# Optimization experiments

Hardware: AMD Instinct MI355X
Metric: run time of the kernel (lower is better)

Reference implementation:

```python
import jax, jax.numpy as jnp
import numpy as np

N, E, B, L = 20000, 320000, 64, 4
DIN_SEQ, DIN_STR, HID = 1280, 128, 256
NHEAD, HDIM = 8, 32
EPS = 1e-5
SLOPE = 0.2


def setup_inputs() -> dict:
    key = jax.random.key(0)
    ks = iter(jax.random.split(key, 64))
    def nrm(shape, scale=0.05):
        return jax.random.normal(next(ks), shape, dtype=jnp.float32) * scale
    return {
        "seq_x": jax.random.normal(next(ks), (N, DIN_SEQ), dtype=jnp.float32),
        "struct_x": jax.random.normal(next(ks), (N, DIN_STR), dtype=jnp.float32),
        "seq_edge_index": jax.random.randint(next(ks), (2, E), 0, N),
        "struct_edge_index": jax.random.randint(next(ks), (2, E), 0, N),
        "seq_batch": jnp.sort(jax.random.randint(next(ks), (N,), 0, B)),
        "struct_batch": jnp.sort(jax.random.randint(next(ks), (N,), 0, B)),
        "seq_proj_W": nrm((DIN_SEQ, HID)), "seq_proj_b": nrm((HID,)),
        "gcn_W": nrm((L, HID, HID)), "gcn_b": nrm((L, HID)),
        "seq_bn_g": jnp.ones((L, HID), jnp.float32), "seq_bn_b": jnp.zeros((L, HID), jnp.float32),
        "struct_proj_W": nrm((DIN_STR, HID)), "struct_proj_b": nrm((HID,)),
        "gat_W": nrm((L, HID, HID)), "gat_att_src": nrm((L, NHEAD, HDIM)),
        "gat_att_dst": nrm((L, NHEAD, HDIM)), "gat_b": nrm((L, HID)),
        "struct_bn_g": jnp.ones((L, HID), jnp.float32), "struct_bn_b": jnp.zeros((L, HID), jnp.float32),
        "Wq": nrm((HID, HID)), "bq": nrm((HID,)),
        "Wk": nrm((HID, HID)), "bk": nrm((HID,)),
        "Wv": nrm((HID, HID)), "bv": nrm((HID,)),
        "Wo": nrm((HID, HID)), "bo": nrm((HID,)),
        "fus_W": nrm((2 * HID, HID)), "fus_b": nrm((HID,)),
        "p1_W": nrm((HID, HID // 2)), "p1_b": nrm((HID // 2,)),
        "p2_W": nrm((HID // 2, 1)), "p2_b": nrm((1,)),
    }


def _add_self_loops(edge_index, n):
    loops = jnp.arange(n, dtype=edge_index.dtype)
    return jnp.concatenate([edge_index[0], loops]), jnp.concatenate([edge_index[1], loops])


def _batchnorm(x, g, b):
    # PyG BatchNorm forward (training-mode batch stats, biased variance, eps=1e-5)
    mu = x.mean(axis=0)
    var = x.var(axis=0)
    return g * (x - mu) * jax.lax.rsqrt(var + EPS) + b


def _gcn(x, src, dst, W, b):
    # GCNConv: symmetric-normalized gather -> scatter-add, self loops already appended
    n = x.shape[0]
    deg = jax.ops.segment_sum(jnp.ones_like(src, dtype=x.dtype), dst, num_segments=n)
    dinv = jax.lax.rsqrt(jnp.maximum(deg, 1.0))
    h = x @ W
    msg = h[src] * (dinv[src] * dinv[dst])[:, None]
    return jax.ops.segment_sum(msg, dst, num_segments=n) + b


def _seg_softmax(e, dst, n):
    m = jax.ops.segment_max(e, dst, num_segments=n)
    ex = jnp.exp(e - m[dst])
    s = jax.ops.segment_sum(ex, dst, num_segments=n)
    return ex / s[dst]


def _gat(x, src, dst, W, a_src, a_dst, b):
    # GATConv: per-edge LeakyReLU attention, softmax over incoming edges, concat heads
    n = x.shape[0]
    h = (x @ W).reshape(n, NHEAD, HDIM)
    e = jax.nn.leaky_relu((h * a_src).sum(-1)[src] + (h * a_dst).sum(-1)[dst], SLOPE)  # [E,H]
    alpha = _seg_softmax(e, dst, n)
    out = jax.ops.segment_sum(h[src] * alpha[:, :, None], dst, num_segments=n)
    return out.reshape(n, NHEAD * HDIM) + b


def _mean_pool(x, batch, nb):
    s = jax.ops.segment_sum(x, batch, num_segments=nb)
    c = jax.ops.segment_sum(jnp.ones((x.shape[0],), x.dtype), batch, num_segments=nb)
    return s / jnp.maximum(c, 1.0)[:, None]


def reference(seq_x, struct_x, seq_edge_index, struct_edge_index, seq_batch, struct_batch,
              seq_proj_W, seq_proj_b, gcn_W, gcn_b, seq_bn_g, seq_bn_b,
              struct_proj_W, struct_proj_b, gat_W, gat_att_src, gat_att_dst, gat_b,
              struct_bn_g, struct_bn_b, Wq, bq, Wk, bk, Wv, bv, Wo, bo,
              fus_W, fus_b, p1_W, p1_b, p2_W, p2_b):
    s_src, s_dst = _add_self_loops(seq_edge_index, seq_x.shape[0])
    t_src, t_dst = _add_self_loops(struct_edge_index, struct_x.shape[0])
    # sequence branch: GCN stack
    xs = jax.nn.relu(seq_x @ seq_proj_W + seq_proj_b)
    for l in range(gcn_W.shape[0]):
        xs = jax.nn.relu(_batchnorm(_gcn(xs, s_src, s_dst, gcn_W[l], gcn_b[l]), seq_bn_g[l], seq_bn_b[l]))
    xs = _mean_pool(xs, seq_batch, B)  # [B, HID]
    # structure branch: GAT stack
    xt = jax.nn.relu(struct_x @ struct_proj_W + struct_proj_b)
    for l in range(gat_W.shape[0]):
        xt = jax.nn.relu(_batchnorm(_gat(xt, t_src, t_dst, gat_W[l], gat_att_src[l], gat_att_dst[l], gat_b[l]), struct_bn_g[l], struct_bn_b[l]))
    xt = _mean_pool(xt, struct_batch, B)  # [B, HID]
    # cross-attention with query/key/value seq-len 1 (softmax over singleton axis)
    q = (xs @ Wq + bq).reshape(B, NHEAD, HDIM)
    k = (xt @ Wk + bk).reshape(B, NHEAD, HDIM)
    v = (xt @ Wv + bv).reshape(B, NHEAD, HDIM)
    scores = (q * k).sum(-1, keepdims=True) * (1.0 / np.sqrt(HDIM))  # [B,H,1]
    attn = jax.nn.softmax(scores, axis=-1)
    x_attn = (attn * v).reshape(B, HID) @ Wo + bo
    # fusion + predictor (dropout inactive at inference)
    xf = jax.nn.relu(jnp.concatenate([x_attn, xt], axis=1) @ fus_W + fus_b)
    h = jax.nn.relu(xf @ p1_W + p1_b)
    return h @ p2_W + p2_b  # [B, 1]
```

## Files before the change

### kernel.cpp

```cpp
#include <hip/hip_runtime.h>
#include <math.h>

#define NN 20000
#define NE 320000
#define NTOT (NE + NN)
#define NBATCH 64
#define HIDW 256
#define NHEADS 8
#define HD 32
#define NL 4
#define BEPS 1e-5f
#define LSLOPE 0.2f
#define WELEMS (128 * HIDW + NL * HIDW * HIDW)

typedef __attribute__((ext_vector_type(8))) short s16x8;
typedef __attribute__((ext_vector_type(8))) unsigned short u16x8;
typedef __attribute__((ext_vector_type(4))) float f32x4;

static __device__ __forceinline__ ushort f2bf(float f) {
  uint u = __float_as_uint(f);
  uint r = (u + 0x7fff + ((u >> 16) & 1)) >> 16;
  return (ushort)r;
}
static __device__ __forceinline__ float bf2f(ushort h) {
  return __uint_as_float(((uint)h) << 16);
}

__global__ __launch_bounds__(1024) void k_scan(const int* __restrict__ cnt,
                                               int* __restrict__ rowptr) {
  __shared__ int tsum[1024];
  int tid = threadIdx.x;
  const int per = (NN + 1023) / 1024;
  int start = tid * per;
  int local = 0;
  for (int j = 0; j < per; ++j) {
    int idx = start + j;
    if (idx < NN) local += cnt[idx];
  }
  tsum[tid] = local;
  __syncthreads();
  for (int off = 1; off < 1024; off <<= 1) {
    int v = (tid >= off) ? tsum[tid - off] : 0;
    __syncthreads();
    tsum[tid] += v;
    __syncthreads();
  }
  int run = (tid == 0) ? 0 : tsum[tid - 1];
  for (int j = 0; j < per; ++j) {
    int idx = start + j;
    if (idx < NN) { rowptr[idx] = run; run += cnt[idx]; }
  }
  if (tid == 1023) rowptr[NN] = tsum[1023];
}

__global__ void k_fill(const int* __restrict__ src, const int* __restrict__ dst,
                       const int* __restrict__ rowptr, int* __restrict__ cur,
                       int* __restrict__ srcs) {
  int i = blockIdx.x * blockDim.x + threadIdx.x;
  if (i >= NTOT) return;
  int s = (i < NE) ? src[i] : (i - NE);
  int d = (i < NE) ? dst[i] : (i - NE);
  int pos = rowptr[d] + atomicAdd(&cur[d], 1);
  srcs[pos] = s;
}

#define WB ((WELEMS + 255) / 256)
#define XB ((NN * 128 / 4 + 255) / 256)
#define HB ((NTOT + 255) / 256)
__global__ __launch_bounds__(256) void k_prep(const float* __restrict__ projW,
                                              const float* __restrict__ gatW,
                                              const float* __restrict__ sx,
                                              const int* __restrict__ e_dst,
                                              ushort* __restrict__ wh,
                                              ushort* __restrict__ sxh,
                                              int* __restrict__ cnt) {
  int bb = blockIdx.x;
  if (bb < WB) {
    int i = bb * 256 + threadIdx.x;
    if (i >= WELEMS) return;
    float v;
    if (i < 128 * HIDW) {
      int n = i >> 7, k = i & 127;
      v = projW[k * HIDW + n];
    } else {
      int j = i - 128 * HIDW;
      int l = j >> 16, r = j & 65535;
      int n = r >> 8, k = r & 255;
      v = gatW[l * 65536 + k * HIDW + n];
    }
    wh[i] = f2bf(v);
  } else if (bb < WB + XB) {
    int idx = (bb - WB) * 256 + threadIdx.x;
    if (idx >= NN * 128 / 4) return;
    int i0 = idx * 4;
    float4 v = *reinterpret_cast<const float4*>(&sx[i0]);
    ushort4 hh;
    hh.x = f2bf(v.x); hh.y = f2bf(v.y); hh.z = f2bf(v.z); hh.w = f2bf(v.w);
    *reinterpret_cast<ushort4*>(&sxh[i0]) = hh;
  } else {
    int i = (bb - WB - XB) * 256 + threadIdx.x;
    if (i >= NTOT) return;
    int d = (i < NE) ? e_dst[i] : (i - NE);
    atomicAdd(&cnt[d], 1);
  }
}

#define ARPB 79
__global__ __launch_bounds__(256) void k_asplit(const ushort* __restrict__ X,
                                                const float* __restrict__ stats64,
                                                const float* __restrict__ g,
                                                const float* __restrict__ b,
                                                ushort* __restrict__ ah) {
  __shared__ float sc_s[HIDW], sh_s[HIDW];
  int c = threadIdx.x;
  float st = 0.f, st2 = 0.f;
  for (int i = 0; i < 64; ++i) {
    st += stats64[(size_t)i * 512 + c];
    st2 += stats64[(size_t)i * 512 + 256 + c];
  }
  float mean = st * (1.f / NN);
  float var = fmaxf(st2 * (1.f / NN) - mean * mean, 0.f);
  float sc = g[c] * rsqrtf(var + BEPS);
  sc_s[c] = sc;
  sh_s[c] = b[c] - mean * sc;
  __syncthreads();
  int r0 = blockIdx.x * ARPB, r1 = min(r0 + ARPB, NN);
  int ch = (c & 31) * 8;
  for (int rb = r0; rb < r1; rb += 8) {
    int r = rb + (c >> 5);
    if (r >= r1) continue;
    u16x8 xin = *reinterpret_cast<const u16x8*>(&X[(size_t)r * HIDW + ch]);
    u16x8 hh;
#pragma unroll
    for (int j = 0; j < 8; ++j) {
      float v = fmaxf(bf2f(xin[j]) * sc_s[ch + j] + sh_s[ch + j], 0.f);
      hh[j] = f2bf(v);
    }
    *reinterpret_cast<u16x8*>(&ah[(size_t)r * HIDW + ch]) = hh;
  }
}

#define GBM 64
#define GBN 64
#define GBK 64
#define NWG 1252
#define SWZ_Q 156
#define SWZ_R 4
__global__ __launch_bounds__(256) void k_mfma(const ushort* __restrict__ Ah,
                                              const ushort* __restrict__ Wh,
                                              const float* __restrict__ bias,
                                              const float* __restrict__ aS,
                                              const float* __restrict__ aD,
                                              ushort* __restrict__ Co,
                                              ushort* __restrict__ Ch,
                                              float* __restrict__ asrc,
                                              float* __restrict__ adst,
                                              int M, int K, int mode) {
  __shared__ __align__(16) ushort As[GBM][72];
  __shared__ __align__(16) ushort Ws[GBN][72];
  int orig = blockIdx.x;
  int xcd = orig & 7, pos = orig >> 3;
  int wgid = (xcd < SWZ_R ? xcd * (SWZ_Q + 1) : SWZ_R * (SWZ_Q + 1) + (xcd - SWZ_R) * SWZ_Q) + pos;
  int rowblk = wgid >> 2, colblk = wgid & 3;
  int row0 = rowblk * GBM, col0 = colblk * GBN;

  int tid = threadIdx.x;
  int wid = tid >> 6, lane = tid & 63;
  int wr = wid >> 1, wc = wid & 1;
  int l15 = lane & 15, l4 = lane >> 4;
  f32x4 acc[2][2] = {};
  int sr = tid >> 2;
  int skq = (tid & 3) * 16;

  for (int k0 = 0; k0 < K; k0 += GBK) {
    int gr = row0 + sr;
    u16x8 va0 = {0,0,0,0,0,0,0,0}, va1 = va0;
    if (gr < M) {
      va0 = *reinterpret_cast<const u16x8*>(&Ah[(size_t)gr * K + k0 + skq]);
      va1 = *reinterpret_cast<const u16x8*>(&Ah[(size_t)gr * K + k0 + skq + 8]);
    }
    u16x8 vw0 = *reinterpret_cast<const u16x8*>(&Wh[(size_t)(col0 + sr) * K + k0 + skq]);
    u16x8 vw1 = *reinterpret_cast<const u16x8*>(&Wh[(size_t)(col0 + sr) * K + k0 + skq + 8]);
    *reinterpret_cast<u16x8*>(&As[sr][skq]) = va0;
    *reinterpret_cast<u16x8*>(&As[sr][skq + 8]) = va1;
    *reinterpret_cast<u16x8*>(&Ws[sr][skq]) = vw0;
    *reinterpret_cast<u16x8*>(&Ws[sr][skq + 8]) = vw1;
    __syncthreads();

#pragma unroll
    for (int ks = 0; ks < 2; ++ks) {
      int ak = ks * 32 + l4 * 8;
      s16x8 af[2], bfv[2];
#pragma unroll
      for (int mf = 0; mf < 2; ++mf)
        af[mf] = *reinterpret_cast<const s16x8*>(&As[wr * 32 + mf * 16 + l15][ak]);
#pragma unroll
      for (int nf = 0; nf < 2; ++nf)
        bfv[nf] = *reinterpret_cast<const s16x8*>(&Ws[wc * 32 + nf * 16 + l15][ak]);
#pragma unroll
      for (int mf = 0; mf < 2; ++mf)
#pragma unroll
        for (int nf = 0; nf < 2; ++nf)
          acc[mf][nf] = __builtin_amdgcn_mfma_f32_16x16x32_bf16(af[mf], bfv[nf], acc[mf][nf], 0, 0, 0);
    }
    __syncthreads();
  }

  if (mode == 0) {
#pragma unroll
    for (int mf = 0; mf < 2; ++mf)
#pragma unroll
      for (int reg = 0; reg < 4; ++reg) {
        int r = row0 + wr * 32 + mf * 16 + l4 * 4 + reg;
        if (r >= M) continue;
#pragma unroll
        for (int nf = 0; nf < 2; ++nf) {
          int c = col0 + wc * 32 + nf * 16 + l15;
          float v = fmaxf(acc[mf][nf][reg] + bias[c], 0.f);
          Co[(size_t)r * HIDW + c] = f2bf(v);
        }
      }
  } else {
    int hg = colblk * 2 + wc;
    float aSv[2], aDv[2];
#pragma unroll
    for (int nf = 0; nf < 2; ++nf) {
      aSv[nf] = aS[hg * HD + nf * 16 + l15];
      aDv[nf] = aD[hg * HD + nf * 16 + l15];
    }
#pragma unroll
    for (int mf = 0; mf < 2; ++mf)
#pragma unroll
      for (int reg = 0; reg < 4; ++reg) {
        int r = row0 + wr * 32 + mf * 16 + l4 * 4 + reg;
        bool ok = (r < M);
        float pa = 0.f, pd = 0.f;
#pragma unroll
        for (int nf = 0; nf < 2; ++nf) {
          float v = acc[mf][nf][reg];
          if (ok) {
            int c = col0 + wc * 32 + nf * 16 + l15;
            Ch[(size_t)r * HIDW + c] = f2bf(v);
          }
          pa += v * aSv[nf];
          pd += v * aDv[nf];
        }
        pa += __shfl_xor(pa, 1); pa += __shfl_xor(pa, 2);
        pa += __shfl_xor(pa, 4); pa += __shfl_xor(pa, 8);
        pd += __shfl_xor(pd, 1); pd += __shfl_xor(pd, 2);
        pd += __shfl_xor(pd, 4); pd += __shfl_xor(pd, 8);
        if (ok && l15 == 0) {
          asrc[r * NHEADS + hg] = pa;
          adst[r * NHEADS + hg] = pd;
        }
      }
  }
}

__global__ __launch_bounds__(256) void k_agg(const ushort* __restrict__ h,
                                             const int* __restrict__ rowptr,
                                             const int* __restrict__ srcs,
                                             const float* __restrict__ asrc,
                                             const float* __restrict__ adst,
                                             ushort* __restrict__ out,
                                             float* __restrict__ stats64) {
  __shared__ float sst[4][512];
  int tid = threadIdx.x;
  int wid = tid >> 6, lane = tid & 63;
  int node = blockIdx.x * 4 + wid;
  int el = lane >> 5, sl = lane & 31;
  int c0 = sl * 8, hh = sl >> 2;
  float adn = adst[node * NHEADS + hh];
  int beg = rowptr[node], end = rowptr[node + 1];
  int deg = end - beg;
  float acc[8] = {};
  float ssum = 0.f;
  for (int w0 = 0; w0 < deg; w0 += 64) {
    int sv = srcs[min(beg + w0 + lane, end - 1)];
    int lim = min(64, deg - w0);
    for (int cb = 0; cb < lim; cb += 16) {
      int s[8];
#pragma unroll
      for (int j = 0; j < 8; ++j) s[j] = __shfl(sv, cb + 2 * j + el);
      float a[8];
      u16x8 hv[8];
#pragma unroll
      for (int j = 0; j < 8; ++j) {
        a[j] = asrc[s[j] * NHEADS + hh];
        hv[j] = *reinterpret_cast<const u16x8*>(&h[(size_t)s[j] * HIDW + c0]);
      }
#pragma unroll
      for (int j = 0; j < 8; ++j) {
        float e = a[j] + adn;
        e = (e >= 0.f) ? e : LSLOPE * e;
        float ex = ((cb + 2 * j + el) < lim) ? __expf(e) : 0.f;
        ssum += ex;
#pragma unroll
        for (int q = 0; q < 8; ++q) acc[q] += ex * bf2f(hv[j][q]);
      }
    }
  }
  ssum += __shfl_xor(ssum, 32);
#pragma unroll
  for (int q = 0; q < 8; ++q) acc[q] += __shfl_xor(acc[q], 32);
  if (el == 0) {
    float inv = 1.f / ssum;
    u16x8 o;
    float of[8];
#pragma unroll
    for (int q = 0; q < 8; ++q) {
      of[q] = acc[q] * inv;
      o[q] = f2bf(of[q]);
    }
    *reinterpret_cast<u16x8*>(&out[(size_t)node * HIDW + c0]) = o;
#pragma unroll
    for (int q = 0; q < 8; ++q) {
      sst[wid][c0 + q] = of[q];
      sst[wid][256 + c0 + q] = of[q] * of[q];
    }
  }
  __syncthreads();
  int c = tid;
  float s = sst[0][c] + sst[1][c] + sst[2][c] + sst[3][c];
  float s2 = sst[0][256 + c] + sst[1][256 + c] + sst[2][256 + c] + sst[3][256 + c];
  float* slice = stats64 + (size_t)(blockIdx.x & 63) * 512;
  atomicAdd(&slice[c], s);
  atomicAdd(&slice[256 + c], s2);
}

__global__ __launch_bounds__(256) void k_pool(const ushort* __restrict__ x,
                                              const float* __restrict__ stats64,
                                              const float* __restrict__ g,
                                              const float* __restrict__ b,
                                              const int* __restrict__ batch,
                                              float* __restrict__ pool,
                                              int* __restrict__ pcnt) {
  int c = threadIdx.x;
  float st = 0.f, st2 = 0.f;
  for (int i = 0; i < 64; ++i) {
    st += stats64[(size_t)i * 512 + c];
    st2 += stats64[(size_t)i * 512 + 256 + c];
  }
  float mean = st * (1.f / NN);
  float var = fmaxf(st2 * (1.f / NN) - mean * mean, 0.f);
  float sc = g[c] * rsqrtf(var + BEPS);
  float sh = b[c] - mean * sc;
  const int RPB = (NN + 255) / 256;
  int r0 = blockIdx.x * RPB, r1 = min(r0 + RPB, NN);
  if (r0 >= r1) return;
  int curb = batch[r0];
  float acc = 0.f;
  int run = 0;
  for (int r = r0; r < r1; ++r) {
    int bb = batch[r];
    if (bb != curb) {
      atomicAdd(&pool[curb * HIDW + c], acc);
      if (c == 0) atomicAdd(&pcnt[curb], run);
      acc = 0.f; run = 0; curb = bb;
    }
    float v = fmaxf(bf2f(x[(size_t)r * HIDW + c]) * sc + sh, 0.f);
    acc += v;
    run++;
  }
  atomicAdd(&pool[curb * HIDW + c], acc);
  if (c == 0) atomicAdd(&pcnt[curb], run);
}

__global__ __launch_bounds__(256) void k_head(const float* __restrict__ pool,
                                              const int* __restrict__ pcnt,
                                              const float* __restrict__ Wv, const float* __restrict__ bv,
                                              const float* __restrict__ Wo, const float* __restrict__ bo,
                                              const float* __restrict__ fusW, const float* __restrict__ fusB,
                                              const float* __restrict__ p1W, const float* __restrict__ p1b,
                                              const float* __restrict__ p2W, const float* __restrict__ p2b,
                                              float* __restrict__ out) {
  __shared__ float pr[HIDW], sA[HIDW], sB[HIDW], sH[128];
  int b = blockIdx.x, c = threadIdx.x;
  float invc = 1.f / fmaxf((float)pcnt[b], 1.f);
  pr[c] = pool[b * HIDW + c] * invc;
  __syncthreads();
  float acc = bv[c];
  for (int k = 0; k < HIDW; ++k) acc += pr[k] * Wv[k * HIDW + c];
  sA[c] = acc;
  __syncthreads();
  acc = bo[c];
  for (int k = 0; k < HIDW; ++k) acc += sA[k] * Wo[k * HIDW + c];
  sB[c] = acc;
  __syncthreads();
  acc = fusB[c];
  for (int k = 0; k < HIDW; ++k) acc += sB[k] * fusW[k * HIDW + c];
  for (int k = 0; k < HIDW; ++k) acc += pr[k] * fusW[(HIDW + k) * HIDW + c];
  float xf = fmaxf(acc, 0.f);
  __syncthreads();
  sA[c] = xf;
  __syncthreads();
  if (c < 128) {
    acc = p1b[c];
    for (int k = 0; k < HIDW; ++k) acc += sA[k] * p1W[k * 128 + c];
    sH[c] = fmaxf(acc, 0.f);
  }
  __syncthreads();
  if (c == 0) {
    float s = p2b[0];
    for (int k = 0; k < 128; ++k) s += sH[k] * p2W[k];
    out[b] = s;
  }
}

extern "C" void kernel_launch(void* const* d_in, const int* in_sizes, int n_in,
                              void* d_out, int out_size, void* d_ws, size_t ws_size,
                              hipStream_t stream) {
  const float* struct_x = (const float*)d_in[1];
  const int* edge = (const int*)d_in[3];
  const int* batch = (const int*)d_in[5];
  const float* projW = (const float*)d_in[12];
  const float* projB = (const float*)d_in[13];
  const float* gatW = (const float*)d_in[14];
  const float* attS = (const float*)d_in[15];
  const float* attD = (const float*)d_in[16];
  const float* bnG = (const float*)d_in[18];
  const float* bnB = (const float*)d_in[19];
  const float* Wv = (const float*)d_in[24];
  const float* bv = (const float*)d_in[25];
  const float* Wo = (const float*)d_in[26];
  const float* bo = (const float*)d_in[27];
  const float* fusW = (const float*)d_in[28];
  const float* fusB = (const float*)d_in[29];
  const float* p1W = (const float*)d_in[30];
  const float* p1b = (const float*)d_in[31];
  const float* p2W = (const float*)d_in[32];
  const float* p2b = (const float*)d_in[33];
  float* out = (float*)d_out;

  const int* e_src = edge;
  const int* e_dst = edge + NE;

  char* ws = (char*)d_ws;
  size_t off = 0;
  auto alloc = [&](size_t bytes) -> void* {
    void* p = ws + off;
    off = (off + bytes + 255) & ~(size_t)255;
    return p;
  };
  ushort* buf0 = (ushort*)alloc((size_t)NN * HIDW * 2);
  ushort* hb = (ushort*)alloc((size_t)NN * HIDW * 2);
  ushort* a0 = (ushort*)alloc((size_t)NN * HIDW * 2);
  ushort* sxh = (ushort*)alloc((size_t)NN * 128 * 2);
  ushort* wth = (ushort*)alloc((size_t)WELEMS * 2);
  int* rowptr = (int*)alloc((NN + 1) * 4);
  int* srcs = (int*)alloc((size_t)NTOT * 4);
  float* asrc = (float*)alloc((size_t)NN * NHEADS * 4);
  float* adst = (float*)alloc((size_t)NN * NHEADS * 4);
  char* zero_base = ws + off;
  int* cnt = (int*)alloc(NN * 4);
  int* cur = (int*)alloc(NN * 4);
  float* stats64 = (float*)alloc((size_t)NL * 64 * 512 * 4);
  float* pool = (float*)alloc(NBATCH * HIDW * 4);
  int* pcnt = (int*)alloc(NBATCH * 4);
  size_t zero_bytes = (ws + off) - zero_base;

  const int TPB = 256;
  const int gEdge = (NTOT + TPB - 1) / TPB;

  hipMemsetAsync(zero_base, 0, zero_bytes, stream);

  k_prep<<<WB + XB + HB, TPB, 0, stream>>>(projW, gatW, struct_x, e_dst, wth, sxh, cnt);
  k_scan<<<1, 1024, 0, stream>>>(cnt, rowptr);
  k_fill<<<gEdge, TPB, 0, stream>>>(e_src, e_dst, rowptr, cur, srcs);

  k_mfma<<<NWG, 256, 0, stream>>>(sxh, wth, projB, nullptr, nullptr,
                                  a0, nullptr, nullptr, nullptr, NN, 128, 0);

  for (int l = 0; l < NL; ++l) {
    const ushort* whL = wth + 128 * HIDW + (size_t)l * HIDW * HIDW;
    float* s64 = stats64 + (size_t)l * 64 * 512;
    k_mfma<<<NWG, 256, 0, stream>>>(a0, whL, nullptr,
                                    attS + l * HIDW, attD + l * HIDW,
                                    nullptr, hb, asrc, adst, NN, HIDW, 1);
    k_agg<<<NN / 4, 256, 0, stream>>>(hb, rowptr, srcs, asrc, adst, buf0, s64);
    if (l < NL - 1) {
      k_asplit<<<(NN + ARPB - 1) / ARPB, TPB, 0, stream>>>(
          buf0, s64, bnG + l * HIDW, bnB + l * HIDW, a0);
    }
  }

  k_pool<<<256, 256, 0, stream>>>(buf0, stats64 + (size_t)3 * 64 * 512,
                                  bnG + 3 * HIDW, bnB + 3 * HIDW, batch, pool, pcnt);

  k_head<<<NBATCH, 256, 0, stream>>>(pool, pcnt, Wv, bv, Wo, bo, fusW, fusB,
                                     p1W, p1b, p2W, p2b, out);
}
```

Before: 333.1 us.

## Fuse batchnorm+relu into GEMM A-load and store GAT features as fp8

Replaces the separate per-layer batchnorm/relu pass with a tiny stats-reduction kernel. The scale and shift are then applied on the fly while the next GEMM loads its A tile, which removes a full read-and-write of the activation matrix. The transformed features fed to the edge aggregation are now stored as fp8 e4m3 instead of bf16, halving the bytes gathered per edge. This trades accuracy for bandwidth, since fp8 has a 3-bit mantissa. It also adds per-element ALU work in the GEMM prologue and an extra small kernel launch per layer.

```diff
diff --git a/kernel.cpp b/kernel.cpp
--- a/kernel.cpp
+++ b/kernel.cpp
@@ -1,4 +1,5 @@
 #include <hip/hip_runtime.h>
+#include <hip/hip_fp8.h>
 #include <math.h>
 
 #define NN 20000
@@ -16,6 +17,7 @@
 typedef __attribute__((ext_vector_type(8))) short s16x8;
 typedef __attribute__((ext_vector_type(8))) unsigned short u16x8;
 typedef __attribute__((ext_vector_type(4))) float f32x4;
+typedef __attribute__((ext_vector_type(2))) unsigned int u32x2;
 
 static __device__ __forceinline__ ushort f2bf(float f) {
   uint u = __float_as_uint(f);
@@ -24,6 +26,15 @@
 }
 static __device__ __forceinline__ float bf2f(ushort h) {
   return __uint_as_float(((uint)h) << 16);
+}
+static __device__ __forceinline__ unsigned char fp8e(float f) {
+  __hip_fp8_e4m3 t(f);
+  return (unsigned char)t.__x;
+}
+static __device__ __forceinline__ float fp8d(unsigned char v) {
+  __hip_fp8_e4m3 t;
+  t.__x = (__hip_fp8_storage_t)v;
+  return (float)t;
 }
 
 __global__ __launch_bounds__(1024) void k_scan(const int* __restrict__ cnt,
@@ -105,13 +116,10 @@
   }
 }
 
-#define ARPB 79
-__global__ __launch_bounds__(256) void k_asplit(const ushort* __restrict__ X,
-                                                const float* __restrict__ stats64,
-                                                const float* __restrict__ g,
-                                                const float* __restrict__ b,
-                                                ushort* __restrict__ ah) {
-  __shared__ float sc_s[HIDW], sh_s[HIDW];
+__global__ __launch_bounds__(256) void k_red(const float* __restrict__ stats64,
+                                             const float* __restrict__ g,
+                                             const float* __restrict__ b,
+                                             float* __restrict__ scsh) {
   int c = threadIdx.x;
   float st = 0.f, st2 = 0.f;
   for (int i = 0; i < 64; ++i) {
@@ -121,23 +129,8 @@
   float mean = st * (1.f / NN);
   float var = fmaxf(st2 * (1.f / NN) - mean * mean, 0.f);
   float sc = g[c] * rsqrtf(var + BEPS);
-  sc_s[c] = sc;
-  sh_s[c] = b[c] - mean * sc;
-  __syncthreads();
-  int r0 = blockIdx.x * ARPB, r1 = min(r0 + ARPB, NN);
-  int ch = (c & 31) * 8;
-  for (int rb = r0; rb < r1; rb += 8) {
-    int r = rb + (c >> 5);
-    if (r >= r1) continue;
-    u16x8 xin = *reinterpret_cast<const u16x8*>(&X[(size_t)r * HIDW + ch]);
-    u16x8 hh;
-#pragma unroll
-    for (int j = 0; j < 8; ++j) {
-      float v = fmaxf(bf2f(xin[j]) * sc_s[ch + j] + sh_s[ch + j], 0.f);
-      hh[j] = f2bf(v);
-    }
-    *reinterpret_cast<u16x8*>(&ah[(size_t)r * HIDW + ch]) = hh;
-  }
+  scsh[c] = sc;
+  scsh[HIDW + c] = b[c] - mean * sc;
 }
 
 #define GBM 64
@@ -148,23 +141,31 @@
 #define SWZ_R 4
 __global__ __launch_bounds__(256) void k_mfma(const ushort* __restrict__ Ah,
                                               const ushort* __restrict__ Wh,
+                                              const float* __restrict__ scshp,
                                               const float* __restrict__ bias,
                                               const float* __restrict__ aS,
                                               const float* __restrict__ aD,
                                               ushort* __restrict__ Co,
-                                              ushort* __restrict__ Ch,
+                                              unsigned char* __restrict__ Ch8,
                                               float* __restrict__ asrc,
                                               float* __restrict__ adst,
                                               int M, int K, int mode) {
   __shared__ __align__(16) ushort As[GBM][72];
   __shared__ __align__(16) ushort Ws[GBN][72];
+  __shared__ float scs[HIDW], shs[HIDW];
+  int tid = threadIdx.x;
+  if (scshp) {
+    scs[tid] = scshp[tid];
+    shs[tid] = scshp[HIDW + tid];
+  }
+  __syncthreads();
+
   int orig = blockIdx.x;
   int xcd = orig & 7, pos = orig >> 3;
   int wgid = (xcd < SWZ_R ? xcd * (SWZ_Q + 1) : SWZ_R * (SWZ_Q + 1) + (xcd - SWZ_R) * SWZ_Q) + pos;
   int rowblk = wgid >> 2, colblk = wgid & 3;
   int row0 = rowblk * GBM, col0 = colblk * GBN;
 
-  int tid = threadIdx.x;
   int wid = tid >> 6, lane = tid & 63;
   int wr = wid >> 1, wc = wid & 1;
   int l15 = lane & 15, l4 = lane >> 4;
@@ -178,6 +179,14 @@
     if (gr < M) {
       va0 = *reinterpret_cast<const u16x8*>(&Ah[(size_t)gr * K + k0 + skq]);
       va1 = *reinterpret_cast<const u16x8*>(&Ah[(size_t)gr * K + k0 + skq + 8]);
+    }
+    if (scshp) {
+      int kcs = k0 + skq;
+#pragma unroll
+      for (int j = 0; j < 8; ++j) {
+        va0[j] = (short)f2bf(fmaxf(bf2f((ushort)va0[j]) * scs[kcs + j] + shs[kcs + j], 0.f));
+        va1[j] = (short)f2bf(fmaxf(bf2f((ushort)va1[j]) * scs[kcs + 8 + j] + shs[kcs + 8 + j], 0.f));
+      }
     }
     u16x8 vw0 = *reinterpret_cast<const u16x8*>(&Wh[(size_t)(col0 + sr) * K + k0 + skq]);
     u16x8 vw1 = *reinterpret_cast<const u16x8*>(&Wh[(size_t)(col0 + sr) * K + k0 + skq + 8]);
@@ -240,7 +249,7 @@
           float v = acc[mf][nf][reg];
           if (ok) {
             int c = col0 + wc * 32 + nf * 16 + l15;
-            Ch[(size_t)r * HIDW + c] = f2bf(v);
+            Ch8[(size_t)r * HIDW + c] = fp8e(v);
           }
           pa += v * aSv[nf];
           pd += v * aDv[nf];
@@ -257,7 +266,7 @@
   }
 }
 
-__global__ __launch_bounds__(256) void k_agg(const ushort* __restrict__ h,
+__global__ __launch_bounds__(256) void k_agg(const unsigned char* __restrict__ h8,
                                              const int* __restrict__ rowptr,
                                              const int* __restrict__ srcs,
                                              const float* __restrict__ asrc,
@@ -283,11 +292,11 @@
 #pragma unroll
       for (int j = 0; j < 8; ++j) s[j] = __shfl(sv, cb + 2 * j + el);
       float a[8];
-      u16x8 hv[8];
+      u32x2 hv[8];
 #pragma unroll
       for (int j = 0; j < 8; ++j) {
         a[j] = asrc[s[j] * NHEADS + hh];
-        hv[j] = *reinterpret_cast<const u16x8*>(&h[(size_t)s[j] * HIDW + c0]);
+        hv[j] = *reinterpret_cast<const u32x2*>(&h8[(size_t)s[j] * HIDW + c0]);
       }
 #pragma unroll
       for (int j = 0; j < 8; ++j) {
@@ -295,8 +304,10 @@
         e = (e >= 0.f) ? e : LSLOPE * e;
         float ex = ((cb + 2 * j + el) < lim) ? __expf(e) : 0.f;
         ssum += ex;
-#pragma unroll
-        for (int q = 0; q < 8; ++q) acc[q] += ex * bf2f(hv[j][q]);
+        union { u32x2 v; unsigned char b[8]; } U;
+        U.v = hv[j];
+#pragma unroll
+        for (int q = 0; q < 8; ++q) acc[q] += ex * fp8d(U.b[q]);
       }
     }
   }
@@ -443,7 +454,7 @@
     return p;
   };
   ushort* buf0 = (ushort*)alloc((size_t)NN * HIDW * 2);
-  ushort* hb = (ushort*)alloc((size_t)NN * HIDW * 2);
+  unsigned char* hb8 = (unsigned char*)alloc((size_t)NN * HIDW);
   ushort* a0 = (ushort*)alloc((size_t)NN * HIDW * 2);
   ushort* sxh = (ushort*)alloc((size_t)NN * 128 * 2);
   ushort* wth = (ushort*)alloc((size_t)WELEMS * 2);
@@ -451,6 +462,7 @@
   int* srcs = (int*)alloc((size_t)NTOT * 4);
   float* asrc = (float*)alloc((size_t)NN * NHEADS * 4);
   float* adst = (float*)alloc((size_t)NN * NHEADS * 4);
+  float* scsh = (float*)alloc(512 * 4);
   char* zero_base = ws + off;
   int* cnt = (int*)alloc(NN * 4);
   int* cur = (int*)alloc(NN * 4);
@@ -468,20 +480,21 @@
   k_scan<<<1, 1024, 0, stream>>>(cnt, rowptr);
   k_fill<<<gEdge, TPB, 0, stream>>>(e_src, e_dst, rowptr, cur, srcs);
 
-  k_mfma<<<NWG, 256, 0, stream>>>(sxh, wth, projB, nullptr, nullptr,
+  k_mfma<<<NWG, 256, 0, stream>>>(sxh, wth, nullptr, projB, nullptr, nullptr,
                                   a0, nullptr, nullptr, nullptr, NN, 128, 0);
 
   for (int l = 0; l < NL; ++l) {
     const ushort* whL = wth + 128 * HIDW + (size_t)l * HIDW * HIDW;
     float* s64 = stats64 + (size_t)l * 64 * 512;
-    k_mfma<<<NWG, 256, 0, stream>>>(a0, whL, nullptr,
+    if (l > 0) {
+      k_red<<<1, 256, 0, stream>>>(stats64 + (size_t)(l - 1) * 64 * 512,
+                                   bnG + (l - 1) * HIDW, bnB + (l - 1) * HIDW, scsh);
+    }
+    k_mfma<<<NWG, 256, 0, stream>>>((l == 0) ? a0 : buf0, whL,
+                                    (l == 0) ? nullptr : scsh, nullptr,
                                     attS + l * HIDW, attD + l * HIDW,
-                                    nullptr, hb, asrc, adst, NN, HIDW, 1);
-    k_agg<<<NN / 4, 256, 0, stream>>>(hb, rowptr, srcs, asrc, adst, buf0, s64);
-    if (l < NL - 1) {
-      k_asplit<<<(NN + ARPB - 1) / ARPB, TPB, 0, stream>>>(
-          buf0, s64, bnG + l * HIDW, bnB + l * HIDW, a0);
-    }
+                                    nullptr, hb8, asrc, adst, NN, HIDW, 1);
+    k_agg<<<NN / 4, 256, 0, stream>>>(hb8, rowptr, srcs, asrc, adst, buf0, s64);
   }
 
   k_pool<<<256, 256, 0, stream>>>(buf0, stats64 + (size_t)3 * 64 * 512,
```

Result: faster. 317.4 us (median of 2 runs) (-4.7%).
